# Kernel tuning notes

Measured on AMD Instinct MI355X. Metric: run time of the kernel, lower is better.

Reference implementation:

```python
import jax, jax.numpy as jnp
import numpy as np
import math

EPS = 1e-07
ALPHA = 0.2
FINAL_LAMBDA = 0.01   # final_beta in the original
ITERATIONS = 2
MEAN_DATA = 1.0

B, H, W, KH, KW, I, O, A = 16, 6, 6, 3, 3, 32, 32, 4


def setup_inputs() -> dict:
    key = jax.random.key(0)
    k1, k2 = jax.random.split(key)
    votes = jax.random.normal(k1, (B, H, W, KH, KW, I, O, A, A), dtype=jnp.float32)
    activations = jax.random.uniform(k2, (B, H, W, KH, KW, I, 1, 1, 1), dtype=jnp.float32)
    beta_a = jnp.full((1, 1, 1, 1, 1, 1, O, 1, 1), 0.5, dtype=jnp.float32)
    beta_u = jnp.full((1, 1, 1, 1, 1, 1, O, 1, 1), 0.5, dtype=jnp.float32)
    return {"votes": votes, "activations": activations, "beta_a": beta_a, "beta_u": beta_u}


def _m_step(a_i, V, R, R_prev, beta_a, beta_u, it_idx):
    # R mixing with previous assignments (faithful to source)
    R = R * a_i * (1.0 - ALPHA) + ALPHA * R_prev
    R_prev = R
    # reduce over kernel (3,4) and input-capsule (5) axes
    sum_R = jnp.sum(R, axis=(3, 4, 5), keepdims=True)                      # (b,h,w,1,1,1,o,1,1)
    mu = jnp.sum(R * V, axis=(3, 4, 5), keepdims=True) / (sum_R + EPS)     # (b,h,w,1,1,1,o,a,a)
    sigma_sq = jnp.sum(R * (V - mu) ** 2, axis=(3, 4, 5), keepdims=True) / (sum_R + EPS)
    cost_h = (beta_u - 0.5 * jnp.log(sigma_sq + EPS)) * sum_R / MEAN_DATA
    inv_temp = FINAL_LAMBDA * (1.0 - 0.95 ** (it_idx + 1))
    a_j = jax.nn.sigmoid(inv_temp * (beta_a - jnp.sum(cost_h, axis=(-1, -2), keepdims=True)))
    return mu, sigma_sq, a_j, R_prev


def _e_step_log(V, mu, sigma_sq, a_j):
    # log-space E-step: log N(V; mu, sigma) summed over the 4x4 pose entries
    log_p = -jnp.sum(jnp.log(2.0 * math.pi * sigma_sq + EPS) + (V - mu) ** 2 / (2.0 * sigma_sq),
                     axis=(-1, -2), keepdims=True)                         # (b,h,w,kh,kw,i,o,1,1)
    log_num = jnp.log(a_j + EPS) + log_p
    log_den = jax.scipy.special.logsumexp(log_num, axis=(3, 4, 6), keepdims=True)
    return jnp.exp(log_num - log_den)


def reference(votes, activations, beta_a, beta_u):
    b, h, w, kh, kw, i, o, a, _ = votes.shape
    # softmax over zeros along axis 6 -> uniform 1/o
    R = jnp.full((b, h, w, 1, 1, i, o, 1, 1), 1.0 / o, dtype=votes.dtype)
    R_prev = R
    mu = sigma_sq = a_j = None
    for it in range(ITERATIONS - 1):
        mu, sigma_sq, a_j, R_prev = _m_step(activations, votes, R, R_prev, beta_a, beta_u, it)
        R = _e_step_log(votes, mu, sigma_sq, a_j)
    # final M-step called with i = iterations (matches source)
    mu, sigma_sq, a_j, R_prev = _m_step(activations, votes, R, R_prev, beta_a, beta_u, ITERATIONS)
    poses = jnp.squeeze(mu, axis=(3, 4, 5))   # (b,h,w,o,a,a)
    acts = jnp.squeeze(a_j, axis=(3, 4, 5))   # (b,h,w,o,1,1)
    return poses, acts
```

## Files before the change

kernel.cpp:

```cpp
#include <hip/hip_runtime.h>


#define KKc 9
#define NIc 32
#define NOc 32
#define NAc 16
#define KIc 288
#define KOc 288
#define NPc 512
#define NSITE 576
#define VSTR 17

#define EPSf 1e-7f
#define TWO_PIf 6.28318530717958647692f

__device__ __forceinline__ float wave_sum(float v) {
#pragma unroll
  for (int off = 32; off; off >>= 1) v += __shfl_down(v, off, 64);
  return v;
}
__device__ __forceinline__ float wave_max(float v) {
#pragma unroll
  for (int off = 32; off; off >>= 1) v = fmaxf(v, __shfl_down(v, off, 64));
  return v;
}

__global__ __launch_bounds__(128)
void em_k1(const float* __restrict__ votes, const float* __restrict__ acts_in,
           const float* __restrict__ beta_a, const float* __restrict__ beta_u,
           float* __restrict__ w_mu1, float* __restrict__ w_i2s,
           float* __restrict__ w_m1v, float* __restrict__ w_m1q,
           float* __restrict__ w_base, float* __restrict__ w_sR1)
{
  const int site = blockIdx.x >> 2;
  const int qtr  = blockIdx.x & 3;
  const int t    = threadIdx.x;
  const int p    = qtr * 128 + t;

  __shared__ float s_act[KIc];
  __shared__ float s_red[2];

  s_act[t] = acts_in[site * KIc + t];
  s_act[t + 128] = acts_in[site * KIc + t + 128];
  if (t < 32) s_act[t + 256] = acts_in[site * KIc + t + 256];
  __syncthreads();

  float v = fmaf(0.8f, s_act[t], 0.2f) + fmaf(0.8f, s_act[t + 128], 0.2f);
  if (t < 32) v += fmaf(0.8f, s_act[t + 256], 0.2f);
  v = wave_sum(v);
  if ((t & 63) == 0) s_red[t >> 6] = v;
  __syncthreads();
  const float sumR1 = (s_red[0] + s_red[1]) * 0.03125f;

  float pv = 0.f, pq = 0.f;
  const float* vs = votes + (size_t)site * (KIc * NPc) + p;
#pragma unroll 8
  for (int ki = 0; ki < KIc; ++ki) {
    const float r = fmaf(0.8f, s_act[ki], 0.2f) * 0.03125f;
    const float x = vs[(size_t)ki * NPc];
    pv = fmaf(r, x, pv);
    pq = fmaf(r, x * x, pq);
  }

  const int o = p >> 4;
  const float sR1e = sumR1 + EPSf;
  const float mu = pv / sR1e;
  const float sg = fmaxf((pq - mu * mu * (sumR1 + 2.f * EPSf)) / sR1e, 0.f);

  w_mu1[(size_t)site * NPc + p] = mu;
  w_i2s[(size_t)site * NPc + p] = 0.5f / sg;
  w_m1v[(size_t)site * NPc + p] = pv;
  w_m1q[(size_t)site * NPc + p] = pq;

  float lt = logf(TWO_PIf * sg + EPSf);
  float ch = (beta_u[o] - 0.5f * logf(sg + EPSf)) * sumR1;
#pragma unroll
  for (int off = 1; off < 16; off <<= 1) {
    ch += __shfl_xor(ch, off, 64);
    lt += __shfl_xor(lt, off, 64);
  }
  if ((t & 15) == 0) {
    const float aj = 1.f / (1.f + expf(-(0.0005f * (beta_a[o] - ch))));
    w_base[site * NOc + o] = logf(aj + EPSf) - lt;
  }
  if (t == 0) w_sR1[site] = sumR1;
}

__global__ __launch_bounds__(256)
void em_k3(const float* __restrict__ votes, const float* __restrict__ acts_in,
           const float* __restrict__ w_mu1, const float* __restrict__ w_i2s,
           const float* __restrict__ w_base,
           float* __restrict__ w_m2v, float* __restrict__ w_m2q,
           float* __restrict__ w_sR2)
{
  const int site = blockIdx.x >> 3;
  const int ig   = blockIdx.x & 7;
  const int t    = threadIdx.x;

  __shared__ float s_V[KOc * VSTR];
  __shared__ float s_mu[NOc * VSTR];
  __shared__ float s_is[NOc * VSTR];
  __shared__ float s_base[NOc];
  __shared__ float s_act[KIc];
  __shared__ float s_w[KOc];
  __shared__ float s_red[4];

  for (int idx = t; idx < NPc; idx += 256) {
    const int o = idx >> 4, a2 = idx & 15;
    s_mu[o * VSTR + a2] = w_mu1[(size_t)site * NPc + idx];
    s_is[o * VSTR + a2] = w_i2s[(size_t)site * NPc + idx];
  }
  if (t < NOc) s_base[t] = w_base[site * NOc + t];
  s_act[t] = acts_in[site * KIc + t];
  if (t < KIc - 256) s_act[t + 256] = acts_in[site * KIc + t + 256];

  const float4* vsite4 = reinterpret_cast<const float4*>(votes + (size_t)site * (KIc * NPc));

  float m2va = 0.f, m2vb = 0.f, m2qa = 0.f, m2qb = 0.f, sR2acc = 0.f;
  const int oB  = t & 31;
  const int a2B = (t >> 5) * 2;

  for (int ii = 0; ii < 4; ++ii) {
    const int i = ig * 4 + ii;
    __syncthreads();
    for (int idx = t; idx < 1152; idx += 256) {
      const int kk  = idx >> 7;
      const int rem = idx & 127;
      const int pair = kk * NOc + (rem >> 2);
      const int a4   = (rem & 3) * 4;
      const float4 x = vsite4[(size_t)(kk * NIc + i) * 128 + rem];
      s_V[pair * VSTR + a4 + 0] = x.x;
      s_V[pair * VSTR + a4 + 1] = x.y;
      s_V[pair * VSTR + a4 + 2] = x.z;
      s_V[pair * VSTR + a4 + 3] = x.w;
    }
    __syncthreads();

    float ln1, ln2 = -1e30f;
    {
      const int o = t & 31;
      float lp = 0.f;
#pragma unroll
      for (int a2 = 0; a2 < NAc; ++a2) {
        const float d = s_V[t * VSTR + a2] - s_mu[o * VSTR + a2];
        lp = fmaf(d * d, s_is[o * VSTR + a2], lp);
      }
      ln1 = s_base[o] - lp;
    }
    if (t < KOc - 256) {
      const int idx = t + 256;
      const int o = idx & 31;
      float lp = 0.f;
#pragma unroll
      for (int a2 = 0; a2 < NAc; ++a2) {
        const float d = s_V[idx * VSTR + a2] - s_mu[o * VSTR + a2];
        lp = fmaf(d * d, s_is[o * VSTR + a2], lp);
      }
      ln2 = s_base[o] - lp;
    }
    float m = wave_max(fmaxf(ln1, ln2));
    if ((t & 63) == 0) s_red[t >> 6] = m;
    __syncthreads();
    m = fmaxf(fmaxf(s_red[0], s_red[1]), fmaxf(s_red[2], s_red[3]));
    float e = expf(ln1 - m) + ((t < KOc - 256) ? expf(ln2 - m) : 0.f);
    e = wave_sum(e);
    __syncthreads();
    if ((t & 63) == 0) s_red[t >> 6] = e;
    __syncthreads();
    const float logden = m + logf(s_red[0] + s_red[1] + s_red[2] + s_red[3]);

    s_w[t] = expf(ln1 - logden) * s_act[(t >> 5) * NIc + i] * 0.8f;
    if (t < KOc - 256)
      s_w[t + 256] = expf(ln2 - logden) * s_act[8 * NIc + i] * 0.8f;
    __syncthreads();

    if (t < NOc) {
      float sw = 0.f;
#pragma unroll
      for (int kk = 0; kk < KKc; ++kk) sw += s_w[kk * NOc + t];
      sR2acc += sw;
    }
#pragma unroll
    for (int kk = 0; kk < KKc; ++kk) {
      const int bb = kk * NOc + oB;
      const float w  = s_w[bb];
      const float va = s_V[bb * VSTR + a2B];
      const float vb = s_V[bb * VSTR + a2B + 1];
      m2va = fmaf(w, va, m2va);
      m2qa = fmaf(w, va * va, m2qa);
      m2vb = fmaf(w, vb, m2vb);
      m2qb = fmaf(w, vb * vb, m2qb);
    }
  }

  reinterpret_cast<float2*>(w_m2v)[(size_t)blockIdx.x * 256 + t] = make_float2(m2va, m2vb);
  reinterpret_cast<float2*>(w_m2q)[(size_t)blockIdx.x * 256 + t] = make_float2(m2qa, m2qb);
  if (t < NOc) w_sR2[(size_t)blockIdx.x * NOc + t] = sR2acc;
}

__global__ __launch_bounds__(256)
void em_k4(const float* __restrict__ beta_a, const float* __restrict__ beta_u,
           const float* __restrict__ w_m1v, const float* __restrict__ w_m1q,
           const float* __restrict__ w_sR1,
           const float* __restrict__ w_m2v, const float* __restrict__ w_m2q,
           const float* __restrict__ w_sR2,
           float* __restrict__ out)
{
  const int site = blockIdx.x;
  const int t    = threadIdx.x;
  const int oB   = t & 31;
  const int a2B  = (t >> 5) * 2;

  __shared__ float s_R[NOc];
  __shared__ float s_c[256];

  float Mva = 0.f, Mvb = 0.f, Mqa = 0.f, Mqb = 0.f, sR2 = 0.f;
#pragma unroll
  for (int g = 0; g < 8; ++g) {
    const size_t blk = (size_t)site * 8 + g;
    const float2 v = reinterpret_cast<const float2*>(w_m2v)[blk * 256 + t];
    const float2 q = reinterpret_cast<const float2*>(w_m2q)[blk * 256 + t];
    Mva += v.x; Mvb += v.y; Mqa += q.x; Mqb += q.y;
    if (t < NOc) sR2 += w_sR2[blk * NOc + t];
  }
  if (t < NOc) s_R[t] = sR2;
  __syncthreads();

  const float sumR1 = w_sR1[site];
  const float sumR  = s_R[oB] + 0.2f * sumR1;
  const float sRe   = sumR + EPSf;
  const int p = oB * NAc + a2B;

  Mva += 0.2f * w_m1v[(size_t)site * NPc + p];
  Mqa += 0.2f * w_m1q[(size_t)site * NPc + p];
  Mvb += 0.2f * w_m1v[(size_t)site * NPc + p + 1];
  Mqb += 0.2f * w_m1q[(size_t)site * NPc + p + 1];

  const float mua = Mva / sRe;
  const float mub = Mvb / sRe;
  const float sga = fmaxf((Mqa - mua * mua * (sumR + 2.f * EPSf)) / sRe, 0.f);
  const float sgb = fmaxf((Mqb - mub * mub * (sumR + 2.f * EPSf)) / sRe, 0.f);

  float* poses = out + (size_t)site * NPc;
  poses[p]     = mua;
  poses[p + 1] = mub;

  const float bu = beta_u[oB];
  s_c[t] = (bu - 0.5f * logf(sga + EPSf)) * sumR
         + (bu - 0.5f * logf(sgb + EPSf)) * sumR;
  __syncthreads();
  if (t < NOc) {
    float c = 0.f;
#pragma unroll
    for (int k = 0; k < 8; ++k) c += s_c[t + 32 * k];
    const float aj = 1.f / (1.f + expf(-(0.00142625f * (beta_a[t] - c))));
    out[(size_t)NSITE * NPc + site * NOc + t] = aj;
  }
}

extern "C" void kernel_launch(void* const* d_in, const int* in_sizes, int n_in,
                              void* d_out, int out_size, void* d_ws, size_t ws_size,
                              hipStream_t stream) {
  const float* votes  = (const float*)d_in[0];
  const float* acts   = (const float*)d_in[1];
  const float* beta_a = (const float*)d_in[2];
  const float* beta_u = (const float*)d_in[3];
  float* out = (float*)d_out;

  float* ws = (float*)d_ws;
  const size_t SP = (size_t)NSITE * NPc;
  float* w_mu1  = ws;
  float* w_i2s  = ws + SP;
  float* w_m1v  = ws + 2 * SP;
  float* w_m1q  = ws + 3 * SP;
  float* w_base = ws + 4 * SP;
  float* w_sR1  = w_base + NSITE * NOc;
  float* w_m2v  = w_sR1 + 1024;
  float* w_m2q  = w_m2v + (size_t)4608 * NPc;
  float* w_sR2  = w_m2q + (size_t)4608 * NPc;

  em_k1<<<NSITE * 4, 128, 0, stream>>>(votes, acts, beta_a, beta_u,
                                       w_mu1, w_i2s, w_m1v, w_m1q, w_base, w_sR1);
  em_k3<<<NSITE * 8, 256, 0, stream>>>(votes, acts, w_mu1, w_i2s, w_base,
                                       w_m2v, w_m2q, w_sR2);
  em_k4<<<NSITE, 256, 0, stream>>>(beta_a, beta_u, w_m1v, w_m1q, w_sR1,
                                   w_m2v, w_m2q, w_sR2, out);
}
```

Before: 562.2 us.

## Restructure EM kernels around per-thread register accumulation and float4 loads

```diff
diff --git a/kernel.cpp b/kernel.cpp
--- a/kernel.cpp
+++ b/kernel.cpp
@@ -6,10 +6,9 @@
 #define NOc 32
 #define NAc 16
 #define KIc 288
-#define KOc 288
 #define NPc 512
 #define NSITE 576
-#define VSTR 17
+#define RSTR 20
 
 #define EPSf 1e-7f
 #define TWO_PIf 6.28318530717958647692f
@@ -35,10 +34,10 @@
   const int site = blockIdx.x >> 2;
   const int qtr  = blockIdx.x & 3;
   const int t    = threadIdx.x;
-  const int p    = qtr * 128 + t;
 
   __shared__ float s_act[KIc];
   __shared__ float s_red[2];
+  __shared__ float s_cr[32 * 9];
 
   s_act[t] = acts_in[site * KIc + t];
   s_act[t + 128] = acts_in[site * KIc + t + 128];
@@ -52,158 +51,197 @@
   __syncthreads();
   const float sumR1 = (s_red[0] + s_red[1]) * 0.03125f;
 
-  float pv = 0.f, pq = 0.f;
-  const float* vs = votes + (size_t)site * (KIc * NPc) + p;
+  const int c  = qtr * 32 + (t & 31);
+  const int r0 = t >> 5;
+  float pv0 = 0.f, pv1 = 0.f, pv2 = 0.f, pv3 = 0.f;
+  float pq0 = 0.f, pq1 = 0.f, pq2 = 0.f, pq3 = 0.f;
+  const float4* vb = reinterpret_cast<const float4*>(votes) + (size_t)site * (KIc * 128) + c;
 #pragma unroll 8
-  for (int ki = 0; ki < KIc; ++ki) {
+  for (int k = 0; k < 72; ++k) {
+    const int ki = r0 + 4 * k;
     const float r = fmaf(0.8f, s_act[ki], 0.2f) * 0.03125f;
-    const float x = vs[(size_t)ki * NPc];
-    pv = fmaf(r, x, pv);
-    pq = fmaf(r, x * x, pq);
-  }
-
-  const int o = p >> 4;
-  const float sR1e = sumR1 + EPSf;
-  const float mu = pv / sR1e;
-  const float sg = fmaxf((pq - mu * mu * (sumR1 + 2.f * EPSf)) / sR1e, 0.f);
-
-  w_mu1[(size_t)site * NPc + p] = mu;
-  w_i2s[(size_t)site * NPc + p] = 0.5f / sg;
-  w_m1v[(size_t)site * NPc + p] = pv;
-  w_m1q[(size_t)site * NPc + p] = pq;
-
-  float lt = logf(TWO_PIf * sg + EPSf);
-  float ch = (beta_u[o] - 0.5f * logf(sg + EPSf)) * sumR1;
-#pragma unroll
-  for (int off = 1; off < 16; off <<= 1) {
-    ch += __shfl_xor(ch, off, 64);
-    lt += __shfl_xor(lt, off, 64);
-  }
-  if ((t & 15) == 0) {
-    const float aj = 1.f / (1.f + expf(-(0.0005f * (beta_a[o] - ch))));
-    w_base[site * NOc + o] = logf(aj + EPSf) - lt;
-  }
-  if (t == 0) w_sR1[site] = sumR1;
+    const float4 x = vb[(size_t)ki * 128];
+    pv0 = fmaf(r, x.x, pv0); pq0 = fmaf(r, x.x * x.x, pq0);
+    pv1 = fmaf(r, x.y, pv1); pq1 = fmaf(r, x.y * x.y, pq1);
+    pv2 = fmaf(r, x.z, pv2); pq2 = fmaf(r, x.z * x.z, pq2);
+    pv3 = fmaf(r, x.w, pv3); pq3 = fmaf(r, x.w * x.w, pq3);
+  }
+  pv0 += __shfl_xor(pv0, 32); pv1 += __shfl_xor(pv1, 32);
+  pv2 += __shfl_xor(pv2, 32); pv3 += __shfl_xor(pv3, 32);
+  pq0 += __shfl_xor(pq0, 32); pq1 += __shfl_xor(pq1, 32);
+  pq2 += __shfl_xor(pq2, 32); pq3 += __shfl_xor(pq3, 32);
+  if (t >= 64 && t < 96) {
+    const int l = t - 64;
+    s_cr[l * 9 + 0] = pv0; s_cr[l * 9 + 1] = pv1; s_cr[l * 9 + 2] = pv2; s_cr[l * 9 + 3] = pv3;
+    s_cr[l * 9 + 4] = pq0; s_cr[l * 9 + 5] = pq1; s_cr[l * 9 + 6] = pq2; s_cr[l * 9 + 7] = pq3;
+  }
+  __syncthreads();
+  if (t < 32) {
+    pv0 += s_cr[t * 9 + 0]; pv1 += s_cr[t * 9 + 1]; pv2 += s_cr[t * 9 + 2]; pv3 += s_cr[t * 9 + 3];
+    pq0 += s_cr[t * 9 + 4]; pq1 += s_cr[t * 9 + 5]; pq2 += s_cr[t * 9 + 6]; pq3 += s_cr[t * 9 + 7];
+
+    const float sR1e = sumR1 + EPSf;
+    const float sR1x = sumR1 + 2.f * EPSf;
+    const float mu0 = pv0 / sR1e, mu1 = pv1 / sR1e, mu2 = pv2 / sR1e, mu3 = pv3 / sR1e;
+    const float sg0 = fmaxf((pq0 - mu0 * mu0 * sR1x) / sR1e, 0.f);
+    const float sg1 = fmaxf((pq1 - mu1 * mu1 * sR1x) / sR1e, 0.f);
+    const float sg2 = fmaxf((pq2 - mu2 * mu2 * sR1x) / sR1e, 0.f);
+    const float sg3 = fmaxf((pq3 - mu3 * mu3 * sR1x) / sR1e, 0.f);
+
+    const size_t fo = (size_t)site * 128 + c;
+    reinterpret_cast<float4*>(w_mu1)[fo] = make_float4(mu0, mu1, mu2, mu3);
+    reinterpret_cast<float4*>(w_i2s)[fo] = make_float4(0.5f / sg0, 0.5f / sg1, 0.5f / sg2, 0.5f / sg3);
+    reinterpret_cast<float4*>(w_m1v)[fo] = make_float4(pv0, pv1, pv2, pv3);
+    reinterpret_cast<float4*>(w_m1q)[fo] = make_float4(pq0, pq1, pq2, pq3);
+
+    const int o = c >> 2;
+    const float bu = beta_u[o];
+    float lt = logf(TWO_PIf * sg0 + EPSf) + logf(TWO_PIf * sg1 + EPSf)
+             + logf(TWO_PIf * sg2 + EPSf) + logf(TWO_PIf * sg3 + EPSf);
+    float ch = (4.f * bu - 0.5f * (logf(sg0 + EPSf) + logf(sg1 + EPSf)
+                                 + logf(sg2 + EPSf) + logf(sg3 + EPSf))) * sumR1;
+    ch += __shfl_xor(ch, 1); ch += __shfl_xor(ch, 2);
+    lt += __shfl_xor(lt, 1); lt += __shfl_xor(lt, 2);
+    if ((t & 3) == 0) {
+      const float aj = 1.f / (1.f + expf(-(0.0005f * (beta_a[o] - ch))));
+      w_base[site * NOc + o] = logf(aj + EPSf) - lt;
+    }
+    if (t == 0) w_sR1[site] = sumR1;
+  }
 }
 
 __global__ __launch_bounds__(256)
 void em_k3(const float* __restrict__ votes, const float* __restrict__ acts_in,
            const float* __restrict__ w_mu1, const float* __restrict__ w_i2s,
-           const float* __restrict__ w_base,
-           float* __restrict__ w_m2v, float* __restrict__ w_m2q,
-           float* __restrict__ w_sR2)
+           const float* __restrict__ w_base, float* __restrict__ w_part)
 {
-  const int site = blockIdx.x >> 3;
+  const int site = (NSITE - 1) - (blockIdx.x >> 3);
   const int ig   = blockIdx.x & 7;
   const int t    = threadIdx.x;
-
-  __shared__ float s_V[KOc * VSTR];
-  __shared__ float s_mu[NOc * VSTR];
-  __shared__ float s_is[NOc * VSTR];
+  const int o    = t & 31;
+
+  __shared__ float s_V[288 * RSTR];
+  __shared__ float s_act[KIc];
   __shared__ float s_base[NOc];
-  __shared__ float s_act[KIc];
-  __shared__ float s_w[KOc];
-  __shared__ float s_red[4];
-
-  for (int idx = t; idx < NPc; idx += 256) {
-    const int o = idx >> 4, a2 = idx & 15;
-    s_mu[o * VSTR + a2] = w_mu1[(size_t)site * NPc + idx];
-    s_is[o * VSTR + a2] = w_i2s[(size_t)site * NPc + idx];
-  }
-  if (t < NOc) s_base[t] = w_base[site * NOc + t];
+  __shared__ float s_rm[4];
+  __shared__ float s_re[4];
+
+  {
+    const int tt = t & 127;
+    const float4 x = reinterpret_cast<const float4*>((t < 128 ? w_mu1 : w_i2s) + (size_t)site * NPc)[tt];
+    float* dst = s_V + (t < 128 ? 0 : 544) + (tt >> 2) * 17 + (tt & 3) * 4;
+    dst[0] = x.x; dst[1] = x.y; dst[2] = x.z; dst[3] = x.w;
+  }
   s_act[t] = acts_in[site * KIc + t];
-  if (t < KIc - 256) s_act[t + 256] = acts_in[site * KIc + t + 256];
-
-  const float4* vsite4 = reinterpret_cast<const float4*>(votes + (size_t)site * (KIc * NPc));
-
-  float m2va = 0.f, m2vb = 0.f, m2qa = 0.f, m2qb = 0.f, sR2acc = 0.f;
-  const int oB  = t & 31;
-  const int a2B = (t >> 5) * 2;
+  if (t < 32) { s_act[256 + t] = acts_in[site * KIc + 256 + t]; s_base[t] = w_base[site * NOc + t]; }
+  __syncthreads();
+  float mu[16], is[16];
+#pragma unroll
+  for (int a = 0; a < 16; ++a) { mu[a] = s_V[o * 17 + a]; is[a] = s_V[544 + o * 17 + a]; }
+  const float lbase = s_base[o];
+  __syncthreads();
+
+  float accv[16], accq[16], accw = 0.f;
+#pragma unroll
+  for (int a = 0; a < 16; ++a) { accv[a] = 0.f; accq[a] = 0.f; }
+
+  const float4* vsl4 = reinterpret_cast<const float4*>(votes) + (size_t)site * (KIc * 128);
 
   for (int ii = 0; ii < 4; ++ii) {
     const int i = ig * 4 + ii;
+#pragma unroll
+    for (int idx = t; idx < 1152; idx += 256) {
+      const int row = idx >> 2;
+      const int a4  = idx & 3;
+      const float4 x = vsl4[(size_t)((row >> 5) * NIc + i) * 128 + (row & 31) * 4 + a4];
+      *reinterpret_cast<float4*>(s_V + row * RSTR + a4 * 4) = x;
+    }
     __syncthreads();
-    for (int idx = t; idx < 1152; idx += 256) {
-      const int kk  = idx >> 7;
-      const int rem = idx & 127;
-      const int pair = kk * NOc + (rem >> 2);
-      const int a4   = (rem & 3) * 4;
-      const float4 x = vsite4[(size_t)(kk * NIc + i) * 128 + rem];
-      s_V[pair * VSTR + a4 + 0] = x.x;
-      s_V[pair * VSTR + a4 + 1] = x.y;
-      s_V[pair * VSTR + a4 + 2] = x.z;
-      s_V[pair * VSTR + a4 + 3] = x.w;
-    }
+
+    float v1[16];
+#pragma unroll
+    for (int j = 0; j < 4; ++j) {
+      const float4 x = *reinterpret_cast<const float4*>(s_V + t * RSTR + 4 * j);
+      v1[4 * j] = x.x; v1[4 * j + 1] = x.y; v1[4 * j + 2] = x.z; v1[4 * j + 3] = x.w;
+    }
+    float lp1 = 0.f;
+#pragma unroll
+    for (int a = 0; a < 16; ++a) { const float d = v1[a] - mu[a]; lp1 = fmaf(d * d, is[a], lp1); }
+    const float ln1 = lbase - lp1;
+
+    float v2[16];
+    float ln2 = -1e30f;
+    if (t < 32) {
+#pragma unroll
+      for (int j = 0; j < 4; ++j) {
+        const float4 x = *reinterpret_cast<const float4*>(s_V + (256 + t) * RSTR + 4 * j);
+        v2[4 * j] = x.x; v2[4 * j + 1] = x.y; v2[4 * j + 2] = x.z; v2[4 * j + 3] = x.w;
+      }
+      float lp2 = 0.f;
+#pragma unroll
+      for (int a = 0; a < 16; ++a) { const float d = v2[a] - mu[a]; lp2 = fmaf(d * d, is[a], lp2); }
+      ln2 = lbase - lp2;
+    }
+
+    float m = wave_max(fmaxf(ln1, ln2));
+    if ((t & 63) == 0) s_rm[t >> 6] = m;
     __syncthreads();
-
-    float ln1, ln2 = -1e30f;
-    {
-      const int o = t & 31;
-      float lp = 0.f;
-#pragma unroll
-      for (int a2 = 0; a2 < NAc; ++a2) {
-        const float d = s_V[t * VSTR + a2] - s_mu[o * VSTR + a2];
-        lp = fmaf(d * d, s_is[o * VSTR + a2], lp);
+    m = fmaxf(fmaxf(s_rm[0], s_rm[1]), fmaxf(s_rm[2], s_rm[3]));
+    float e = expf(ln1 - m) + ((t < 32) ? expf(ln2 - m) : 0.f);
+    e = wave_sum(e);
+    if ((t & 63) == 0) s_re[t >> 6] = e;
+    __syncthreads();
+    const float logden = m + logf(s_re[0] + s_re[1] + s_re[2] + s_re[3]);
+
+    const float w1 = expf(ln1 - logden) * s_act[(t >> 5) * NIc + i] * 0.8f;
+    accw += w1;
+#pragma unroll
+    for (int a = 0; a < 16; ++a) {
+      accv[a] = fmaf(w1, v1[a], accv[a]);
+      accq[a] = fmaf(w1, v1[a] * v1[a], accq[a]);
+    }
+    if (t < 32) {
+      const float w2 = expf(ln2 - logden) * s_act[8 * NIc + i] * 0.8f;
+      accw += w2;
+#pragma unroll
+      for (int a = 0; a < 16; ++a) {
+        accv[a] = fmaf(w2, v2[a], accv[a]);
+        accq[a] = fmaf(w2, v2[a] * v2[a], accq[a]);
       }
-      ln1 = s_base[o] - lp;
-    }
-    if (t < KOc - 256) {
-      const int idx = t + 256;
-      const int o = idx & 31;
-      float lp = 0.f;
-#pragma unroll
-      for (int a2 = 0; a2 < NAc; ++a2) {
-        const float d = s_V[idx * VSTR + a2] - s_mu[o * VSTR + a2];
-        lp = fmaf(d * d, s_is[o * VSTR + a2], lp);
+    }
+  }
+
+  accw += __shfl_xor(accw, 32);
+#pragma unroll
+  for (int a = 0; a < 16; ++a) {
+    accv[a] += __shfl_xor(accv[a], 32);
+    accq[a] += __shfl_xor(accq[a], 32);
+  }
+  float* s_p = s_V;
+  {
+    const int l = t & 63, wv = t >> 6;
+    if (l < 32) {
+#pragma unroll
+      for (int a = 0; a < 16; ++a) {
+        s_p[a * 128 + wv * 32 + l] = accv[a];
+        s_p[(16 + a) * 128 + wv * 32 + l] = accq[a];
       }
-      ln2 = s_base[o] - lp;
-    }
-    float m = wave_max(fmaxf(ln1, ln2));
-    if ((t & 63) == 0) s_red[t >> 6] = m;
-    __syncthreads();
-    m = fmaxf(fmaxf(s_red[0], s_red[1]), fmaxf(s_red[2], s_red[3]));
-    float e = expf(ln1 - m) + ((t < KOc - 256) ? expf(ln2 - m) : 0.f);
-    e = wave_sum(e);
-    __syncthreads();
-    if ((t & 63) == 0) s_red[t >> 6] = e;
-    __syncthreads();
-    const float logden = m + logf(s_red[0] + s_red[1] + s_red[2] + s_red[3]);
-
-    s_w[t] = expf(ln1 - logden) * s_act[(t >> 5) * NIc + i] * 0.8f;
-    if (t < KOc - 256)
-      s_w[t + 256] = expf(ln2 - logden) * s_act[8 * NIc + i] * 0.8f;
-    __syncthreads();
-
-    if (t < NOc) {
-      float sw = 0.f;
-#pragma unroll
-      for (int kk = 0; kk < KKc; ++kk) sw += s_w[kk * NOc + t];
-      sR2acc += sw;
-    }
-#pragma unroll
-    for (int kk = 0; kk < KKc; ++kk) {
-      const int bb = kk * NOc + oB;
-      const float w  = s_w[bb];
-      const float va = s_V[bb * VSTR + a2B];
-      const float vb = s_V[bb * VSTR + a2B + 1];
-      m2va = fmaf(w, va, m2va);
-      m2qa = fmaf(w, va * va, m2qa);
-      m2vb = fmaf(w, vb, m2vb);
-      m2qb = fmaf(w, vb * vb, m2qb);
-    }
-  }
-
-  reinterpret_cast<float2*>(w_m2v)[(size_t)blockIdx.x * 256 + t] = make_float2(m2va, m2vb);
-  reinterpret_cast<float2*>(w_m2q)[(size_t)blockIdx.x * 256 + t] = make_float2(m2qa, m2qb);
-  if (t < NOc) w_sR2[(size_t)blockIdx.x * NOc + t] = sR2acc;
+      s_p[32 * 128 + wv * 32 + l] = accw;
+    }
+  }
+  __syncthreads();
+  float* wp = w_part + (size_t)(site * 8 + ig) * (33 * 32);
+  for (int j = t >> 5; j < 33; j += 8) {
+    const float s = s_p[j * 128 + o] + s_p[j * 128 + 32 + o]
+                  + s_p[j * 128 + 64 + o] + s_p[j * 128 + 96 + o];
+    wp[j * 32 + o] = s;
+  }
 }
 
 __global__ __launch_bounds__(256)
 void em_k4(const float* __restrict__ beta_a, const float* __restrict__ beta_u,
            const float* __restrict__ w_m1v, const float* __restrict__ w_m1q,
-           const float* __restrict__ w_sR1,
-           const float* __restrict__ w_m2v, const float* __restrict__ w_m2q,
-           const float* __restrict__ w_sR2,
+           const float* __restrict__ w_sR1, const float* __restrict__ w_part,
            float* __restrict__ out)
 {
   const int site = blockIdx.x;
@@ -211,39 +249,35 @@
   const int oB   = t & 31;
   const int a2B  = (t >> 5) * 2;
 
-  __shared__ float s_R[NOc];
+  __shared__ float s_M[33 * 32];
   __shared__ float s_c[256];
 
-  float Mva = 0.f, Mvb = 0.f, Mqa = 0.f, Mqb = 0.f, sR2 = 0.f;
-#pragma unroll
-  for (int g = 0; g < 8; ++g) {
-    const size_t blk = (size_t)site * 8 + g;
-    const float2 v = reinterpret_cast<const float2*>(w_m2v)[blk * 256 + t];
-    const float2 q = reinterpret_cast<const float2*>(w_m2q)[blk * 256 + t];
-    Mva += v.x; Mvb += v.y; Mqa += q.x; Mqb += q.y;
-    if (t < NOc) sR2 += w_sR2[blk * NOc + t];
-  }
-  if (t < NOc) s_R[t] = sR2;
+  for (int j = t >> 5; j < 33; j += 8) {
+    float s = 0.f;
+#pragma unroll
+    for (int g = 0; g < 8; ++g)
+      s += w_part[(size_t)(site * 8 + g) * (33 * 32) + j * 32 + oB];
+    s_M[j * 32 + oB] = s;
+  }
   __syncthreads();
 
   const float sumR1 = w_sR1[site];
-  const float sumR  = s_R[oB] + 0.2f * sumR1;
+  const float sumR  = s_M[32 * 32 + oB] + 0.2f * sumR1;
   const float sRe   = sumR + EPSf;
+  const float sRx   = sumR + 2.f * EPSf;
   const int p = oB * NAc + a2B;
 
-  Mva += 0.2f * w_m1v[(size_t)site * NPc + p];
-  Mqa += 0.2f * w_m1q[(size_t)site * NPc + p];
-  Mvb += 0.2f * w_m1v[(size_t)site * NPc + p + 1];
-  Mqb += 0.2f * w_m1q[(size_t)site * NPc + p + 1];
+  const float Mva = s_M[a2B * 32 + oB]        + 0.2f * w_m1v[(size_t)site * NPc + p];
+  const float Mvb = s_M[(a2B + 1) * 32 + oB]  + 0.2f * w_m1v[(size_t)site * NPc + p + 1];
+  const float Mqa = s_M[(16 + a2B) * 32 + oB] + 0.2f * w_m1q[(size_t)site * NPc + p];
+  const float Mqb = s_M[(17 + a2B) * 32 + oB] + 0.2f * w_m1q[(size_t)site * NPc + p + 1];
 
   const float mua = Mva / sRe;
   const float mub = Mvb / sRe;
-  const float sga = fmaxf((Mqa - mua * mua * (sumR + 2.f * EPSf)) / sRe, 0.f);
-  const float sgb = fmaxf((Mqb - mub * mub * (sumR + 2.f * EPSf)) / sRe, 0.f);
-
-  float* poses = out + (size_t)site * NPc;
-  poses[p]     = mua;
-  poses[p + 1] = mub;
+  const float sga = fmaxf((Mqa - mua * mua * sRx) / sRe, 0.f);
+  const float sgb = fmaxf((Mqb - mub * mub * sRx) / sRe, 0.f);
+
+  reinterpret_cast<float2*>(out + (size_t)site * NPc)[p >> 1] = make_float2(mua, mub);
 
   const float bu = beta_u[oB];
   s_c[t] = (bu - 0.5f * logf(sga + EPSf)) * sumR
@@ -275,14 +309,10 @@
   float* w_m1q  = ws + 3 * SP;
   float* w_base = ws + 4 * SP;
   float* w_sR1  = w_base + NSITE * NOc;
-  float* w_m2v  = w_sR1 + 1024;
-  float* w_m2q  = w_m2v + (size_t)4608 * NPc;
-  float* w_sR2  = w_m2q + (size_t)4608 * NPc;
+  float* w_part = w_sR1 + 1024;
 
   em_k1<<<NSITE * 4, 128, 0, stream>>>(votes, acts, beta_a, beta_u,
                                        w_mu1, w_i2s, w_m1v, w_m1q, w_base, w_sR1);
-  em_k3<<<NSITE * 8, 256, 0, stream>>>(votes, acts, w_mu1, w_i2s, w_base,
-                                       w_m2v, w_m2q, w_sR2);
-  em_k4<<<NSITE, 256, 0, stream>>>(beta_a, beta_u, w_m1v, w_m1q, w_sR1,
-                                   w_m2v, w_m2q, w_sR2, out);
-}
+  em_k3<<<NSITE * 8, 256, 0, stream>>>(votes, acts, w_mu1, w_i2s, w_base, w_part);
+  em_k4<<<NSITE, 256, 0, stream>>>(beta_a, beta_u, w_m1v, w_m1q, w_sR1, w_part, out);
+}
```

Result: no change. 554.6 us (-1.3%).
